# Kernel tuning notes

Hardware: AMD Instinct MI355X
Metric: run time of the kernel (lower is better)

## Reference

```python
import jax, jax.numpy as jnp
import numpy as np

B, S, H = 2, 2048, 2048
NH, NKV, HD = 16, 4, 128
ROPE_BASE = 10000.0


def hbit_linear(x, w):
    # BitNet: 8-bit per-token absmax activation quant, ternary (2-bit) weight quant
    s = 127.0 / jnp.clip(jnp.max(jnp.abs(x), axis=-1, keepdims=True), 1e-5, None)
    xq = jnp.clip(jnp.round(x * s), -128, 127) / s
    ws = 1.0 / jnp.clip(jnp.mean(jnp.abs(w)), 1e-5, None)
    wq = jnp.clip(jnp.round(w * ws), -1, 1) / ws
    return xq @ wq.T


def rotate_half(x):
    h = x.shape[-1] // 2
    return jnp.concatenate([-x[..., h:], x[..., :h]], axis=-1)


def rope_cos_sin(position_ids, head_dim, dtype):
    inv_freq = 1.0 / (ROPE_BASE ** (jnp.arange(0, head_dim, 2, dtype=jnp.float32) / head_dim))
    freqs = position_ids.astype(jnp.float32)[..., None] * inv_freq[None, None, :]  # (b,s,hd/2)
    emb = jnp.concatenate([freqs, freqs], axis=-1)  # (b,s,hd)
    return jnp.cos(emb).astype(dtype)[:, :, None, :], jnp.sin(emb).astype(dtype)[:, :, None, :]


def setup_inputs() -> dict:
    key = jax.random.key(0)
    ks = jax.random.split(key, 5)
    xavier = lambda k, shp: jax.random.uniform(k, shp, jnp.float32, -1.0, 1.0) * np.sqrt(6.0 / (shp[0] + shp[1]))
    causal = jnp.where(jnp.tril(jnp.ones((S, S), bool)), 0.0, -1e9).astype(jnp.float32)[None, None]
    return {
        "hidden_states": jax.random.normal(ks[0], (B, S, H), jnp.float32),
        "attention_mask": causal,
        "Wq": xavier(ks[1], (H, H)),
        "Wk": xavier(ks[2], (NKV * HD, H)),
        "Wv": xavier(ks[3], (NKV * HD, H)),
        "Wo": xavier(ks[4], (H, H)),
        "position_ids": jnp.arange(S, dtype=jnp.int64 if jax.config.jax_enable_x64 else jnp.int32)[None, :],
    }


def reference(hidden_states, attention_mask, Wq, Wk, Wv, Wo, position_ids):
    b, s, _ = hidden_states.shape
    q = hbit_linear(hidden_states, Wq).reshape(b, s, NH, HD)
    k = hbit_linear(hidden_states, Wk).reshape(b, s, NKV, HD)
    v = hbit_linear(hidden_states, Wv).reshape(b, s, NKV, HD)
    cos, sin = rope_cos_sin(position_ids, HD, q.dtype)  # (1,s,1,hd)
    q = q * cos + rotate_half(q) * sin
    k = k * cos + rotate_half(k) * sin
    n_rep = NH // NKV
    k = jnp.repeat(k, n_rep, axis=2)  # (b,s,NH,hd)
    v = jnp.repeat(v, n_rep, axis=2)
    scale = 1.0 / np.sqrt(HD)
    scores = jnp.einsum("bqhd,bkhd->bhqk", q, k) * scale + attention_mask
    probs = jax.nn.softmax(scores, axis=-1)  # dropout inactive (eval)
    out = jnp.einsum("bhqk,bkhd->bqhd", probs, v).reshape(b, s, NH * HD)
    return hbit_linear(out, Wo)
```

## Files before the change

kernel.cpp:

```cpp
#include <hip/hip_runtime.h>
#include <hip/hip_bf16.h>

#define B_ 2
#define S_ 2048
#define H_ 2048
#define NH_ 16
#define NKV_ 4
#define HD_ 128
#define M_ (B_*S_)
#define KVD_ (NKV_*HD_)

typedef signed char s8;
typedef __attribute__((ext_vector_type(8))) short short8;
typedef __attribute__((ext_vector_type(4))) float f32x4;
typedef __attribute__((ext_vector_type(4))) int int4v;

__device__ __forceinline__ float loadf(const void* p, long i, int isb){
  if (isb) return __bfloat162float(((const __hip_bfloat16*)p)[i]);
  return ((const float*)p)[i];
}

__device__ __forceinline__ unsigned short f2bf(float f){
  union { float f; unsigned u; } v; v.f = f;
  unsigned r = v.u + 0x7FFF + ((v.u >> 16) & 1);
  return (unsigned short)(r >> 16);
}

__device__ __forceinline__ float bf2f(unsigned short b){
  union { unsigned u; float f; } v; v.u = ((unsigned)b) << 16; return v.f;
}

__device__ __forceinline__ void gl2lds16(const void* g, void* l){
  __builtin_amdgcn_global_load_lds(
      (const __attribute__((address_space(1))) void*)g,
      (__attribute__((address_space(3))) void*)l, 16, 0, 0);
}

__global__ void k_detect(const unsigned int* x, int* flag){
  __shared__ int sh[256];
  int t = threadIdx.x, c = 0;
  for (int i = t; i < 2048; i += 256){
    unsigned e = (x[i] >> 7) & 0xFF;
    if (e >= 90 && e <= 150) c++;
  }
  sh[t] = c; __syncthreads();
  for (int k = 128; k > 0; k >>= 1){ if (t < k) sh[t] += sh[t+k]; __syncthreads(); }
  if (t == 0) flag[0] = (sh[0] > 1228) ? 1 : 0;
}

__global__ void k_rope_tab(float* ct, float* st){
  int d = threadIdx.x, pos = blockIdx.x;
  float inv = exp2f(-(float)d * 0.20762050593045952f);
  float a = (float)pos * inv;
  float sn, cs; sincosf(a, &sn, &cs);
  ct[pos*64 + d] = cs; st[pos*64 + d] = sn;
}

__global__ void k_wsum_all(const void* Wq, const void* Wk, const void* Wv, const void* Wo,
                           const int* flag, float* wsum){
  __shared__ float sh[256];
  int isb = *flag;
  int bid = blockIdx.x, t = threadIdx.x;
  const void* w; long n; int wi; long b0; int nb;
  if (bid < 512)       { w = Wq; wi = 0; n = (long)H_*H_;   b0 = bid;      nb = 512; }
  else if (bid < 768)  { w = Wk; wi = 1; n = (long)KVD_*H_; b0 = bid-512;  nb = 256; }
  else if (bid < 1024) { w = Wv; wi = 2; n = (long)KVD_*H_; b0 = bid-768;  nb = 256; }
  else                 { w = Wo; wi = 3; n = (long)H_*H_;   b0 = bid-1024; nb = 512; }
  float s = 0.f;
  for (long i = b0*256 + t; i < n; i += (long)nb*256) s += fabsf(loadf(w, i, isb));
  sh[t] = s; __syncthreads();
  for (int k = 128; k > 0; k >>= 1){ if (t < k) sh[t] += sh[t+k]; __syncthreads(); }
  if (t == 0) atomicAdd(&wsum[wi], sh[0]);
}

__global__ void k_wfin(const float* wsum, float* wscale){
  const float cnt[4] = { (float)((long)H_*H_), (float)((long)KVD_*H_),
                         (float)((long)KVD_*H_), (float)((long)H_*H_) };
  int t = threadIdx.x;
  if (t < 4){
    float m = wsum[t] / cnt[t];
    m = fmaxf(m, 1e-5f);
    wscale[t] = 1.0f / m;
  }
}

__global__ void k_wquant_all(const void* Wq, const void* Wk, const void* Wv, const void* Wo,
                             const int* flag, const float* wscale,
                             s8* oq, s8* ok, s8* ov, s8* oo){
  int isb = *flag;
  int bid = blockIdx.x, t = threadIdx.x;
  const void* w; s8* out; long n; int wi; long b0; int nb;
  if (bid < 1024)      { w = Wq; out = oq; wi = 0; n = (long)H_*H_;   b0 = bid;       nb = 1024; }
  else if (bid < 1280) { w = Wk; out = ok; wi = 1; n = (long)KVD_*H_; b0 = bid-1024;  nb = 256; }
  else if (bid < 1536) { w = Wv; out = ov; wi = 2; n = (long)KVD_*H_; b0 = bid-1280;  nb = 256; }
  else                 { w = Wo; out = oo; wi = 3; n = (long)H_*H_;   b0 = bid-1536;  nb = 1024; }
  float sc = wscale[wi];
  for (long i = b0*256 + t; i < n; i += (long)nb*256){
    float v = rintf(loadf(w, i, isb) * sc);
    v = fminf(fmaxf(v, -1.f), 1.f);
    out[i] = (s8)v;
  }
}

__global__ void k_aquant_in(const void* x, const int* flag, float* srow, s8* xq){
  __shared__ float sh[256];
  int isb = *flag; int r = blockIdx.x, t = threadIdx.x;
  long base = (long)r * H_;
  float v[8];
  if (isb){
    uint4 wv = ((const uint4*)((const unsigned short*)x + base))[t];
    unsigned u[4] = {wv.x, wv.y, wv.z, wv.w};
    #pragma unroll
    for (int i = 0; i < 4; i++){
      v[2*i]   = bf2f((unsigned short)(u[i] & 0xFFFF));
      v[2*i+1] = bf2f((unsigned short)(u[i] >> 16));
    }
  } else {
    const float4* p = (const float4*)((const float*)x + base);
    float4 a = p[t*2], b2 = p[t*2+1];
    v[0]=a.x; v[1]=a.y; v[2]=a.z; v[3]=a.w; v[4]=b2.x; v[5]=b2.y; v[6]=b2.z; v[7]=b2.w;
  }
  float mx = 0.f;
  #pragma unroll
  for (int i = 0; i < 8; i++) mx = fmaxf(mx, fabsf(v[i]));
  sh[t] = mx; __syncthreads();
  for (int k = 128; k > 0; k >>= 1){ if (t < k) sh[t] = fmaxf(sh[t], sh[t+k]); __syncthreads(); }
  float s = 127.0f / fmaxf(sh[0], 1e-5f);
  if (t == 0) srow[r] = s;
  unsigned long long pk = 0;
  #pragma unroll
  for (int i = 0; i < 8; i++){
    float q = fminf(fmaxf(rintf(v[i] * s), -128.f), 127.f);
    pk |= ((unsigned long long)(unsigned char)(s8)q) << (8*i);
  }
  *(unsigned long long*)(xq + base + t*8) = pk;
}

__global__ void k_aquant_f32(const float* x, float* srow, s8* xq){
  __shared__ float sh[256];
  int r = blockIdx.x, t = threadIdx.x;
  long base = (long)r * H_;
  const float4* p = (const float4*)(x + base);
  float4 a = p[t*2], b2 = p[t*2+1];
  float v[8] = {a.x,a.y,a.z,a.w,b2.x,b2.y,b2.z,b2.w};
  float mx = 0.f;
  #pragma unroll
  for (int i = 0; i < 8; i++) mx = fmaxf(mx, fabsf(v[i]));
  sh[t] = mx; __syncthreads();
  for (int k = 128; k > 0; k >>= 1){ if (t < k) sh[t] = fmaxf(sh[t], sh[t+k]); __syncthreads(); }
  float s = 127.0f / fmaxf(sh[0], 1e-5f);
  if (t == 0) srow[r] = s;
  unsigned long long pk = 0;
  #pragma unroll
  for (int i = 0; i < 8; i++){
    float q = fminf(fmaxf(rintf(v[i] * s), -128.f), 127.f);
    pk |= ((unsigned long long)(unsigned char)(s8)q) << (8*i);
  }
  *(unsigned long long*)(xq + base + t*8) = pk;
}

__global__ __launch_bounds__(256, 2) void k_gemm_mfma2(
      const s8* __restrict__ A, const s8* __restrict__ Bw,
      const float* __restrict__ srow, const float* __restrict__ wscale, int wi,
      void* __restrict__ Cout, int N, int mode,
      const int* __restrict__ flag, unsigned short* __restrict__ Vt,
      const float* __restrict__ ct, const float* __restrict__ st){
  __shared__ __align__(16) s8 As[128*64];
  __shared__ __align__(16) s8 Bs[128*64];
  int tid = threadIdx.x;
  int wave = tid >> 6, lane = tid & 63;
  int quad = lane >> 4, c = lane & 15;
  int wm = wave >> 1, wn = wave & 1;
  long arow = (long)blockIdx.y * 128, bcol = (long)blockIdx.x * 128;
  const int K = H_;

  int4v acc[4][4];
  #pragma unroll
  for (int mt = 0; mt < 4; mt++)
    #pragma unroll
    for (int nt = 0; nt < 4; nt++) acc[mt][nt] = (int4v){0,0,0,0};

  int rl = lane >> 2;
  int kq = (lane & 3) ^ ((lane >> 3) & 3);
  int ch0 = wave*2, ch1 = wave*2 + 1;
  long gA0 = (arow + ch0*16 + rl)*(long)K + kq*16;
  long gA1 = (arow + ch1*16 + rl)*(long)K + kq*16;
  long gB0 = (bcol + ch0*16 + rl)*(long)K + kq*16;
  long gB1 = (bcol + ch1*16 + rl)*(long)K + kq*16;

  int sA = quad ^ ((c >> 1) & 3);
  int ntl[4];
  #pragma unroll
  for (int nt = 0; nt < 4; nt++) ntl[nt] = 2*wn + (nt & 1) + 4*(nt >> 1);
  int frA[4], frB[4];
  #pragma unroll
  for (int mt = 0; mt < 4; mt++) frA[mt] = (wm*64 + mt*16 + c)*64 + sA*16;
  #pragma unroll
  for (int nt = 0; nt < 4; nt++) frB[nt] = (ntl[nt]*16 + c)*64 + sA*16;

  for (int k0 = 0; k0 < K; k0 += 64){
    gl2lds16(A  + gA0 + k0, As + ch0*1024);
    gl2lds16(A  + gA1 + k0, As + ch1*1024);
    gl2lds16(Bw + gB0 + k0, Bs + ch0*1024);
    gl2lds16(Bw + gB1 + k0, Bs + ch1*1024);
    __syncthreads();
    int4v afr[4], bfr[4];
    #pragma unroll
    for (int mt = 0; mt < 4; mt++) afr[mt] = *(const int4v*)&As[frA[mt]];
    #pragma unroll
    for (int nt = 0; nt < 4; nt++) bfr[nt] = *(const int4v*)&Bs[frB[nt]];
    #pragma unroll
    for (int mt = 0; mt < 4; mt++)
      #pragma unroll
      for (int nt = 0; nt < 4; nt++)
        acc[mt][nt] = __builtin_amdgcn_mfma_i32_16x16x64_i8(afr[mt], bfr[nt], acc[mt][nt], 0, 0, 0);
    __syncthreads();
  }

  float wsc = wscale[wi];
  if (mode == 0 || mode == 3){
    unsigned short* Ob = (unsigned short*)Cout;
    #pragma unroll
    for (int mt = 0; mt < 4; mt++){
      #pragma unroll
      for (int r = 0; r < 4; r++){
        long grow = arow + wm*64 + mt*16 + quad*4 + r;
        float sc = 1.0f / (srow[grow] * wsc);
        if (mode == 0) sc *= 0.08838834764831845f;
        int pos = (int)(grow & (S_-1));
        #pragma unroll
        for (int p = 0; p < 2; p++){
          int col_lo = (int)bcol + (2*wn + p)*16 + c;
          int d = col_lo & 63;
          float cv = ct[pos*64 + d], sv = st[pos*64 + d];
          float vlo = acc[mt][p][r]   * sc;
          float vhi = acc[mt][p+2][r] * sc;
          Ob[grow*(long)N + col_lo]      = f2bf(vlo*cv - vhi*sv);
          Ob[grow*(long)N + col_lo + 64] = f2bf(vhi*cv + vlo*sv);
        }
      }
    }
  } else if (mode == 1){
    #pragma unroll
    for (int mt = 0; mt < 4; mt++){
      #pragma unroll
      for (int r = 0; r < 4; r++){
        long grow = arow + wm*64 + mt*16 + quad*4 + r;
        float sc = 1.0f / (srow[grow] * wsc);
        long bb = grow >> 11; int sI = (int)(grow & (S_-1));
        unsigned short* base = Vt + bb*(long)KVD_*S_ + sI;
        #pragma unroll
        for (int nt = 0; nt < 4; nt++)
          base[(long)(bcol + ntl[nt]*16 + c)*S_] = f2bf(acc[mt][nt][r] * sc);
      }
    }
  } else {
    #pragma unroll
    for (int mt = 0; mt < 4; mt++){
      #pragma unroll
      for (int r = 0; r < 4; r++){
        long grow = arow + wm*64 + mt*16 + quad*4 + r;
        float sc = 1.0f / (srow[grow] * wsc);
        long cb = grow*(long)N + bcol + c;
        if (*flag){
          __hip_bfloat16* o = (__hip_bfloat16*)Cout;
          #pragma unroll
          for (int nt = 0; nt < 4; nt++)
            o[cb + ntl[nt]*16] = __float2bfloat16(acc[mt][nt][r] * sc);
        } else {
          float* o = (float*)Cout;
          #pragma unroll
          for (int nt = 0; nt < 4; nt++)
            o[cb + ntl[nt]*16] = acc[mt][nt][r] * sc;
        }
      }
    }
  }
}

#define PSTR 40
__global__ __launch_bounds__(256) void k_attn_mfma(const unsigned short* __restrict__ Qb,
    const unsigned short* __restrict__ Kb, const unsigned short* __restrict__ Vt,
    float* __restrict__ ob){
  int wid = threadIdx.x >> 6, lane = threadIdx.x & 63;
  int quad = lane >> 4, c = lane & 15;
  int kvh = blockIdx.y, b = blockIdx.z;
  int win = blockIdx.x;
  if (b == 1) win = (S_/32 - 1) - win;
  int h = kvh*4 + wid;
  int q0 = win*32;

  __shared__ __align__(16) unsigned short Ks[64*128];
  __shared__ __align__(16) unsigned short Vs[128*64];
  __shared__ __align__(16) unsigned short Ps[4][16*PSTR];

  short8 qf[2][4];
  #pragma unroll
  for (int t0 = 0; t0 < 2; t0++)
    #pragma unroll
    for (int f = 0; f < 4; f++)
      qf[t0][f] = *(const short8*)(Qb + ((long)(b*S_ + q0 + t0*16 + c)*NH_ + h)*HD_ + f*32 + quad*8);

  const unsigned short* Kg = Kb + (long)b*S_*KVD_ + kvh*HD_;
  const unsigned short* Vg = Vt + ((long)b*KVD_ + kvh*HD_)*S_;

  f32x4 o[2][8], ol[2];
  #pragma unroll
  for (int t0 = 0; t0 < 2; t0++){
    #pragma unroll
    for (int i = 0; i < 8; i++) o[t0][i] = (f32x4){0.f,0.f,0.f,0.f};
    ol[t0] = (f32x4){0.f,0.f,0.f,0.f};
  }
  short8 ones;
  #pragma unroll
  for (int i = 0; i < 8; i++) ones[i] = (short)0x3F80;

  int skey = lane >> 4;
  int kslot = lane & 15;
  int vrow = lane >> 3;
  int vslot = lane & 7;

  int nk = q0 + 32;
  for (int kc = 0; kc < nk; kc += 64){
    #pragma unroll
    for (int i = 0; i < 4; i++){
      int kk = wid*16 + i*4;
      int key = kk + skey;
      int g = kslot ^ (key & 15);
      gl2lds16(Kg + (long)(kc + key)*KVD_ + g*8, Ks + kk*128);
    }
    #pragma unroll
    for (int i = 0; i < 4; i++){
      int rr = wid*32 + i*8;
      int hd = rr + vrow;
      int g = vslot ^ (hd & 7);
      gl2lds16(Vg + (long)hd*S_ + kc + g*8, Vs + rr*64);
    }
    __syncthreads();

    f32x4 s[2][4];
    #pragma unroll
    for (int t0 = 0; t0 < 2; t0++)
      #pragma unroll
      for (int kt = 0; kt < 4; kt++) s[t0][kt] = (f32x4){0.f,0.f,0.f,0.f};
    #pragma unroll
    for (int kt = 0; kt < 4; kt++){
      short8 kf4[4];
      #pragma unroll
      for (int f = 0; f < 4; f++)
        kf4[f] = *(const short8*)&Ks[(kt*16 + c)*128 + ((f*4 + quad) ^ c)*8];
      #pragma unroll
      for (int t0 = 0; t0 < 2; t0++)
        #pragma unroll
        for (int f = 0; f < 4; f++)
          s[t0][kt] = __builtin_amdgcn_mfma_f32_16x16x32_bf16(qf[t0][f], kf4[f], s[t0][kt], 0, 0, 0);
    }
    #pragma unroll
    for (int t0 = 0; t0 < 2; t0++){
      int qr0 = q0 + t0*16;
      if (kc + 63 > qr0){
        #pragma unroll
        for (int kt = 0; kt < 4; kt++){
          int key = kc + kt*16 + c;
          #pragma unroll
          for (int r = 0; r < 4; r++)
            if (key > qr0 + quad*4 + r) s[t0][kt][r] = -1e30f;
        }
      }
    }
    #pragma unroll
    for (int pp = 0; pp < 2; pp++){
      short8 vf[8];
      #pragma unroll
      for (int nt = 0; nt < 8; nt++)
        vf[nt] = *(const short8*)&Vs[(nt*16 + c)*64 + ((pp*4 + quad) ^ (c & 7))*8];
      #pragma unroll
      for (int t0 = 0; t0 < 2; t0++){
        #pragma unroll
        for (int tk = 0; tk < 2; tk++)
          #pragma unroll
          for (int r = 0; r < 4; r++)
            Ps[wid][(quad*4 + r)*PSTR + tk*16 + c] = f2bf(__expf(s[t0][pp*2 + tk][r]));
        short8 pf = *(const short8*)&Ps[wid][c*PSTR + quad*8];
        #pragma unroll
        for (int nt = 0; nt < 8; nt++)
          o[t0][nt] = __builtin_amdgcn_mfma_f32_16x16x32_bf16(pf, vf[nt], o[t0][nt], 0, 0, 0);
        ol[t0] = __builtin_amdgcn_mfma_f32_16x16x32_bf16(pf, ones, ol[t0], 0, 0, 0);
      }
    }
    __syncthreads();
  }

  #pragma unroll
  for (int t0 = 0; t0 < 2; t0++){
    float il[4];
    #pragma unroll
    for (int r = 0; r < 4; r++) il[r] = 1.0f / ol[t0][r];
    #pragma unroll
    for (int nt = 0; nt < 8; nt++)
      #pragma unroll
      for (int r = 0; r < 4; r++)
        ob[((long)(b*S_ + q0 + t0*16 + quad*4 + r))*H_ + h*HD_ + nt*16 + c] = o[t0][nt][r]*il[r];
  }
}

extern "C" void kernel_launch(void* const* d_in, const int* in_sizes, int n_in,
                              void* d_out, int out_size, void* d_ws, size_t ws_size,
                              hipStream_t stream){
  (void)in_sizes; (void)n_in; (void)out_size; (void)ws_size;
  const void* x  = d_in[0];
  const void* Wq = d_in[2];
  const void* Wk = d_in[3];
  const void* Wv = d_in[4];
  const void* Wo = d_in[5];
  char* ws = (char*)d_ws;
  size_t o = 0;
  auto alloc = [&](size_t b){ size_t r = o; o += (b + 255) & ~(size_t)255; return r; };
  size_t META = alloc(256);
  float* wsum   = (float*)(ws + META);
  float* wscale = (float*)(ws + META + 16);
  int*   flag   = (int*)  (ws + META + 32);
  float* s_x = (float*)(ws + alloc((size_t)M_*4));
  float* s_a = (float*)(ws + alloc((size_t)M_*4));
  float* ct  = (float*)(ws + alloc((size_t)S_*64*4));
  float* st  = (float*)(ws + alloc((size_t)S_*64*4));
  s8* xq  = (s8*)(ws + alloc((size_t)M_*H_));
  s8* wqq = (s8*)(ws + alloc((size_t)H_*H_));
  s8* wkq = (s8*)(ws + alloc((size_t)KVD_*H_));
  s8* wvq = (s8*)(ws + alloc((size_t)KVD_*H_));
  s8* woq = (s8*)(ws + alloc((size_t)H_*H_));
  unsigned short* Qb = (unsigned short*)(ws + alloc((size_t)M_*NH_*HD_*2));
  unsigned short* Kb = (unsigned short*)(ws + alloc((size_t)M_*KVD_*2));
  unsigned short* Vt = (unsigned short*)(ws + alloc((size_t)M_*KVD_*2));
  float* ab = (float*)(ws + alloc((size_t)M_*H_*4));
  s8* aq = xq;

  hipMemsetAsync(ws + META, 0, 64, stream);
  k_detect<<<1,256,0,stream>>>((const unsigned int*)x, flag);
  k_rope_tab<<<S_,64,0,stream>>>(ct, st);

  k_wsum_all<<<1536,256,0,stream>>>(Wq, Wk, Wv, Wo, flag, wsum);
  k_wfin<<<1,64,0,stream>>>(wsum, wscale);
  k_wquant_all<<<2560,256,0,stream>>>(Wq, Wk, Wv, Wo, flag, wscale, wqq, wkq, wvq, woq);

  k_aquant_in<<<M_,256,0,stream>>>(x, flag, s_x, xq);

  dim3 gq(H_/128, M_/128), gkv(KVD_/128, M_/128);
  k_gemm_mfma2<<<gq, 256, 0, stream>>>(xq, wqq, s_x, wscale, 0, Qb, H_,   0, flag, nullptr, ct, st);
  k_gemm_mfma2<<<gkv,256, 0, stream>>>(xq, wkq, s_x, wscale, 1, Kb, KVD_, 3, flag, nullptr, ct, st);
  k_gemm_mfma2<<<gkv,256, 0, stream>>>(xq, wvq, s_x, wscale, 2, nullptr, KVD_, 1, flag, Vt, ct, st);

  dim3 ga(S_/32, NKV_, B_);
  k_attn_mfma<<<ga, 256, 0, stream>>>(Qb, Kb, Vt, ab);

  k_aquant_f32<<<M_,256,0,stream>>>(ab, s_a, aq);
  k_gemm_mfma2<<<gq,256,0,stream>>>(aq, woq, s_a, wscale, 3, d_out, H_, 2, flag, nullptr, ct, st);
}
```

Measured before the change: 353.0 us.

## Fuse prep kernels, merge QKV GEMMs, double-buffer K in attention, bf16 attention output

Merges the rope-table, weight-sum and weight-scale kernels into fewer launches. It also folds the Q, K and V projections into one GEMM launch with a block-index dispatch, and double-buffers K tiles in the attention loop so the next chunk loads during softmax·V. The attention output is now written as bf16 instead of fp32, halving its traffic for the activation-quant step. The bf16 rounding before 8-bit quantization can shift a few quantized values.

```diff
diff --git a/kernel.cpp b/kernel.cpp
--- a/kernel.cpp
+++ b/kernel.cpp
@@ -48,24 +48,22 @@
   if (t == 0) flag[0] = (sh[0] > 1228) ? 1 : 0;
 }
 
-__global__ void k_rope_tab(float* ct, float* st){
-  int d = threadIdx.x, pos = blockIdx.x;
-  float inv = exp2f(-(float)d * 0.20762050593045952f);
-  float a = (float)pos * inv;
-  float sn, cs; sincosf(a, &sn, &cs);
-  ct[pos*64 + d] = cs; st[pos*64 + d] = sn;
-}
-
-__global__ void k_wsum_all(const void* Wq, const void* Wk, const void* Wv, const void* Wo,
-                           const int* flag, float* wsum){
+__global__ void k_prep(const void* Wq, const void* Wk, const void* Wv, const void* Wo,
+                       const int* flag, float* wsum, float* ct, float* st){
+  int bid = blockIdx.x, t = threadIdx.x;
+  if (t < 64){
+    float inv = exp2f(-(float)t * 0.20762050593045952f);
+    float a = (float)bid * inv;
+    float sn, cs; sincosf(a, &sn, &cs);
+    ct[bid*64 + t] = cs; st[bid*64 + t] = sn;
+  }
   __shared__ float sh[256];
   int isb = *flag;
-  int bid = blockIdx.x, t = threadIdx.x;
   const void* w; long n; int wi; long b0; int nb;
-  if (bid < 512)       { w = Wq; wi = 0; n = (long)H_*H_;   b0 = bid;      nb = 512; }
-  else if (bid < 768)  { w = Wk; wi = 1; n = (long)KVD_*H_; b0 = bid-512;  nb = 256; }
-  else if (bid < 1024) { w = Wv; wi = 2; n = (long)KVD_*H_; b0 = bid-768;  nb = 256; }
-  else                 { w = Wo; wi = 3; n = (long)H_*H_;   b0 = bid-1024; nb = 512; }
+  if (bid < 768)       { w = Wq; wi = 0; n = (long)H_*H_;   b0 = bid;      nb = 768; }
+  else if (bid < 1024) { w = Wk; wi = 1; n = (long)KVD_*H_; b0 = bid-768;  nb = 256; }
+  else if (bid < 1280) { w = Wv; wi = 2; n = (long)KVD_*H_; b0 = bid-1024; nb = 256; }
+  else                 { w = Wo; wi = 3; n = (long)H_*H_;   b0 = bid-1280; nb = 768; }
   float s = 0.f;
   for (long i = b0*256 + t; i < n; i += (long)nb*256) s += fabsf(loadf(w, i, isb));
   sh[t] = s; __syncthreads();
@@ -73,28 +71,19 @@
   if (t == 0) atomicAdd(&wsum[wi], sh[0]);
 }
 
-__global__ void k_wfin(const float* wsum, float* wscale){
-  const float cnt[4] = { (float)((long)H_*H_), (float)((long)KVD_*H_),
-                         (float)((long)KVD_*H_), (float)((long)H_*H_) };
-  int t = threadIdx.x;
-  if (t < 4){
-    float m = wsum[t] / cnt[t];
-    m = fmaxf(m, 1e-5f);
-    wscale[t] = 1.0f / m;
-  }
-}
-
 __global__ void k_wquant_all(const void* Wq, const void* Wk, const void* Wv, const void* Wo,
-                             const int* flag, const float* wscale,
+                             const int* flag, const float* wsum,
                              s8* oq, s8* ok, s8* ov, s8* oo){
   int isb = *flag;
   int bid = blockIdx.x, t = threadIdx.x;
-  const void* w; s8* out; long n; int wi; long b0; int nb;
-  if (bid < 1024)      { w = Wq; out = oq; wi = 0; n = (long)H_*H_;   b0 = bid;       nb = 1024; }
-  else if (bid < 1280) { w = Wk; out = ok; wi = 1; n = (long)KVD_*H_; b0 = bid-1024;  nb = 256; }
-  else if (bid < 1536) { w = Wv; out = ov; wi = 2; n = (long)KVD_*H_; b0 = bid-1280;  nb = 256; }
-  else                 { w = Wo; out = oo; wi = 3; n = (long)H_*H_;   b0 = bid-1536;  nb = 1024; }
-  float sc = wscale[wi];
+  const float cntq = (float)((long)H_*H_), cntkv = (float)((long)KVD_*H_);
+  const void* w; s8* out; long n; int wi; long b0; int nb; float cnt;
+  if (bid < 1024)      { w = Wq; out = oq; wi = 0; n = (long)H_*H_;   b0 = bid;       nb = 1024; cnt = cntq; }
+  else if (bid < 1280) { w = Wk; out = ok; wi = 1; n = (long)KVD_*H_; b0 = bid-1024;  nb = 256;  cnt = cntkv; }
+  else if (bid < 1536) { w = Wv; out = ov; wi = 2; n = (long)KVD_*H_; b0 = bid-1280;  nb = 256;  cnt = cntkv; }
+  else                 { w = Wo; out = oo; wi = 3; n = (long)H_*H_;   b0 = bid-1536;  nb = 1024; cnt = cntq; }
+  float mean = fmaxf(wsum[wi] / cnt, 1e-5f);
+  float sc = 1.0f / mean;
   for (long i = b0*256 + t; i < n; i += (long)nb*256){
     float v = rintf(loadf(w, i, isb) * sc);
     v = fminf(fmaxf(v, -1.f), 1.f);
@@ -136,13 +125,18 @@
   *(unsigned long long*)(xq + base + t*8) = pk;
 }
 
-__global__ void k_aquant_f32(const float* x, float* srow, s8* xq){
+__global__ void k_aquant_bf16(const unsigned short* __restrict__ x, float* __restrict__ srow, s8* __restrict__ xq){
   __shared__ float sh[256];
   int r = blockIdx.x, t = threadIdx.x;
   long base = (long)r * H_;
-  const float4* p = (const float4*)(x + base);
-  float4 a = p[t*2], b2 = p[t*2+1];
-  float v[8] = {a.x,a.y,a.z,a.w,b2.x,b2.y,b2.z,b2.w};
+  uint4 wv = ((const uint4*)(x + base))[t];
+  unsigned u[4] = {wv.x, wv.y, wv.z, wv.w};
+  float v[8];
+  #pragma unroll
+  for (int i = 0; i < 4; i++){
+    v[2*i]   = bf2f((unsigned short)(u[i] & 0xFFFF));
+    v[2*i+1] = bf2f((unsigned short)(u[i] >> 16));
+  }
   float mx = 0.f;
   #pragma unroll
   for (int i = 0; i < 8; i++) mx = fmaxf(mx, fabsf(v[i]));
@@ -159,19 +153,17 @@
   *(unsigned long long*)(xq + base + t*8) = pk;
 }
 
-__global__ __launch_bounds__(256, 2) void k_gemm_mfma2(
-      const s8* __restrict__ A, const s8* __restrict__ Bw,
-      const float* __restrict__ srow, const float* __restrict__ wscale, int wi,
-      void* __restrict__ Cout, int N, int mode,
-      const int* __restrict__ flag, unsigned short* __restrict__ Vt,
-      const float* __restrict__ ct, const float* __restrict__ st){
-  __shared__ __align__(16) s8 As[128*64];
-  __shared__ __align__(16) s8 Bs[128*64];
+__device__ __forceinline__ void gemm_core(
+      const s8* __restrict__ A, const s8* __restrict__ Bw, s8* As, s8* Bs,
+      const float* __restrict__ srow, float mean,
+      void* __restrict__ Cout, int N, int mode, int isb,
+      unsigned short* __restrict__ Vt,
+      const float* __restrict__ ct, const float* __restrict__ st, long bcol){
   int tid = threadIdx.x;
   int wave = tid >> 6, lane = tid & 63;
   int quad = lane >> 4, c = lane & 15;
   int wm = wave >> 1, wn = wave & 1;
-  long arow = (long)blockIdx.y * 128, bcol = (long)blockIdx.x * 128;
+  long arow = (long)blockIdx.y * 128;
   const int K = H_;
 
   int4v acc[4][4];
@@ -217,7 +209,6 @@
     __syncthreads();
   }
 
-  float wsc = wscale[wi];
   if (mode == 0 || mode == 3){
     unsigned short* Ob = (unsigned short*)Cout;
     #pragma unroll
@@ -225,7 +216,7 @@
       #pragma unroll
       for (int r = 0; r < 4; r++){
         long grow = arow + wm*64 + mt*16 + quad*4 + r;
-        float sc = 1.0f / (srow[grow] * wsc);
+        float sc = mean / srow[grow];
         if (mode == 0) sc *= 0.08838834764831845f;
         int pos = (int)(grow & (S_-1));
         #pragma unroll
@@ -246,7 +237,7 @@
       #pragma unroll
       for (int r = 0; r < 4; r++){
         long grow = arow + wm*64 + mt*16 + quad*4 + r;
-        float sc = 1.0f / (srow[grow] * wsc);
+        float sc = mean / srow[grow];
         long bb = grow >> 11; int sI = (int)(grow & (S_-1));
         unsigned short* base = Vt + bb*(long)KVD_*S_ + sI;
         #pragma unroll
@@ -260,9 +251,9 @@
       #pragma unroll
       for (int r = 0; r < 4; r++){
         long grow = arow + wm*64 + mt*16 + quad*4 + r;
-        float sc = 1.0f / (srow[grow] * wsc);
+        float sc = mean / srow[grow];
         long cb = grow*(long)N + bcol + c;
-        if (*flag){
+        if (isb){
           __hip_bfloat16* o = (__hip_bfloat16*)Cout;
           #pragma unroll
           for (int nt = 0; nt < 4; nt++)
@@ -278,10 +269,44 @@
   }
 }
 
+__global__ __launch_bounds__(256, 2) void k_gemm_qkv(
+      const s8* __restrict__ xq,
+      const s8* __restrict__ wqq, const s8* __restrict__ wkq, const s8* __restrict__ wvq,
+      const float* __restrict__ srow, const float* __restrict__ wsum,
+      unsigned short* __restrict__ Qb, unsigned short* __restrict__ Kb,
+      unsigned short* __restrict__ Vt,
+      const float* __restrict__ ct, const float* __restrict__ st){
+  __shared__ __align__(16) s8 As[128*64];
+  __shared__ __align__(16) s8 Bs[128*64];
+  int bx = blockIdx.x;
+  const float cntq = (float)((long)H_*H_), cntkv = (float)((long)KVD_*H_);
+  const s8* Bw; void* Cout; unsigned short* vt = nullptr;
+  int N, mode; float mean; long bcol;
+  if (bx < 16){
+    Bw = wqq; Cout = Qb; N = H_;   mode = 0; mean = fmaxf(wsum[0]/cntq, 1e-5f);  bcol = (long)bx*128;
+  } else if (bx < 20){
+    Bw = wkq; Cout = Kb; N = KVD_; mode = 3; mean = fmaxf(wsum[1]/cntkv, 1e-5f); bcol = (long)(bx-16)*128;
+  } else {
+    Bw = wvq; Cout = nullptr; vt = Vt; N = KVD_; mode = 1; mean = fmaxf(wsum[2]/cntkv, 1e-5f); bcol = (long)(bx-20)*128;
+  }
+  gemm_core(xq, Bw, As, Bs, srow, mean, Cout, N, mode, 0, vt, ct, st, bcol);
+}
+
+__global__ __launch_bounds__(256, 2) void k_gemm_o(
+      const s8* __restrict__ aq, const s8* __restrict__ woq,
+      const float* __restrict__ srow, const float* __restrict__ wsum,
+      const int* __restrict__ flag, void* __restrict__ out,
+      const float* __restrict__ ct, const float* __restrict__ st){
+  __shared__ __align__(16) s8 As[128*64];
+  __shared__ __align__(16) s8 Bs[128*64];
+  float mean = fmaxf(wsum[3] / (float)((long)H_*H_), 1e-5f);
+  gemm_core(aq, woq, As, Bs, srow, mean, out, H_, 2, *flag, nullptr, ct, st, (long)blockIdx.x*128);
+}
+
 #define PSTR 40
 __global__ __launch_bounds__(256) void k_attn_mfma(const unsigned short* __restrict__ Qb,
     const unsigned short* __restrict__ Kb, const unsigned short* __restrict__ Vt,
-    float* __restrict__ ob){
+    unsigned short* __restrict__ ob){
   int wid = threadIdx.x >> 6, lane = threadIdx.x & 63;
   int quad = lane >> 4, c = lane & 15;
   int kvh = blockIdx.y, b = blockIdx.z;
@@ -290,7 +315,7 @@
   int h = kvh*4 + wid;
   int q0 = win*32;
 
-  __shared__ __align__(16) unsigned short Ks[64*128];
+  __shared__ __align__(16) unsigned short Ks[2][64*128];
   __shared__ __align__(16) unsigned short Vs[128*64];
   __shared__ __align__(16) unsigned short Ps[4][16*PSTR];
 
@@ -321,22 +346,24 @@
   int vslot = lane & 7;
 
   int nk = q0 + 32;
-  for (int kc = 0; kc < nk; kc += 64){
-    #pragma unroll
-    for (int i = 0; i < 4; i++){
-      int kk = wid*16 + i*4;
-      int key = kk + skey;
-      int g = kslot ^ (key & 15);
-      gl2lds16(Kg + (long)(kc + key)*KVD_ + g*8, Ks + kk*128);
-    }
+  #pragma unroll
+  for (int i = 0; i < 4; i++){
+    int kk = wid*16 + i*4;
+    int key = kk + skey;
+    int g = kslot ^ (key & 15);
+    gl2lds16(Kg + (long)key*KVD_ + g*8, &Ks[0][kk*128]);
+  }
+
+  int buf = 0;
+  for (int kc = 0; kc < nk; kc += 64, buf ^= 1){
+    __syncthreads();
     #pragma unroll
     for (int i = 0; i < 4; i++){
       int rr = wid*32 + i*8;
       int hd = rr + vrow;
       int g = vslot ^ (hd & 7);
-      gl2lds16(Vg + (long)hd*S_ + kc + g*8, Vs + rr*64);
-    }
-    __syncthreads();
+      gl2lds16(Vg + (long)hd*S_ + kc + g*8, &Vs[rr*64]);
+    }
 
     f32x4 s[2][4];
     #pragma unroll
@@ -348,7 +375,7 @@
       short8 kf4[4];
       #pragma unroll
       for (int f = 0; f < 4; f++)
-        kf4[f] = *(const short8*)&Ks[(kt*16 + c)*128 + ((f*4 + quad) ^ c)*8];
+        kf4[f] = *(const short8*)&Ks[buf][(kt*16 + c)*128 + ((f*4 + quad) ^ c)*8];
       #pragma unroll
       for (int t0 = 0; t0 < 2; t0++)
         #pragma unroll
@@ -368,6 +395,19 @@
         }
       }
     }
+
+    __syncthreads();
+
+    if (kc + 64 < nk){
+      #pragma unroll
+      for (int i = 0; i < 4; i++){
+        int kk = wid*16 + i*4;
+        int key = kk + skey;
+        int g = kslot ^ (key & 15);
+        gl2lds16(Kg + (long)(kc + 64 + key)*KVD_ + g*8, &Ks[buf^1][kk*128]);
+      }
+    }
+
     #pragma unroll
     for (int pp = 0; pp < 2; pp++){
       short8 vf[8];
@@ -388,7 +428,6 @@
         ol[t0] = __builtin_amdgcn_mfma_f32_16x16x32_bf16(pf, ones, ol[t0], 0, 0, 0);
       }
     }
-    __syncthreads();
   }
 
   #pragma unroll
@@ -400,7 +439,7 @@
     for (int nt = 0; nt < 8; nt++)
       #pragma unroll
       for (int r = 0; r < 4; r++)
-        ob[((long)(b*S_ + q0 + t0*16 + quad*4 + r))*H_ + h*HD_ + nt*16 + c] = o[t0][nt][r]*il[r];
+        ob[((long)(b*S_ + q0 + t0*16 + quad*4 + r))*H_ + h*HD_ + nt*16 + c] = f2bf(o[t0][nt][r]*il[r]);
   }
 }
 
@@ -417,9 +456,8 @@
   size_t o = 0;
   auto alloc = [&](size_t b){ size_t r = o; o += (b + 255) & ~(size_t)255; return r; };
   size_t META = alloc(256);
-  float* wsum   = (float*)(ws + META);
-  float* wscale = (float*)(ws + META + 16);
-  int*   flag   = (int*)  (ws + META + 32);
+  float* wsum = (float*)(ws + META);
+  int*   flag = (int*)  (ws + META + 32);
   float* s_x = (float*)(ws + alloc((size_t)M_*4));
   float* s_a = (float*)(ws + alloc((size_t)M_*4));
   float* ct  = (float*)(ws + alloc((size_t)S_*64*4));
@@ -432,27 +470,23 @@
   unsigned short* Qb = (unsigned short*)(ws + alloc((size_t)M_*NH_*HD_*2));
   unsigned short* Kb = (unsigned short*)(ws + alloc((size_t)M_*KVD_*2));
   unsigned short* Vt = (unsigned short*)(ws + alloc((size_t)M_*KVD_*2));
-  float* ab = (float*)(ws + alloc((size_t)M_*H_*4));
+  unsigned short* ab = (unsigned short*)(ws + alloc((size_t)M_*H_*2));
   s8* aq = xq;
 
   hipMemsetAsync(ws + META, 0, 64, stream);
   k_detect<<<1,256,0,stream>>>((const unsigned int*)x, flag);
-  k_rope_tab<<<S_,64,0,stream>>>(ct, st);
-
-  k_wsum_all<<<1536,256,0,stream>>>(Wq, Wk, Wv, Wo, flag, wsum);
-  k_wfin<<<1,64,0,stream>>>(wsum, wscale);
-  k_wquant_all<<<2560,256,0,stream>>>(Wq, Wk, Wv, Wo, flag, wscale, wqq, wkq, wvq, woq);
-
+  k_prep<<<2048,256,0,stream>>>(Wq, Wk, Wv, Wo, flag, wsum, ct, st);
+  k_wquant_all<<<2560,256,0,stream>>>(Wq, Wk, Wv, Wo, flag, wsum, wqq, wkq, wvq, woq);
   k_aquant_in<<<M_,256,0,stream>>>(x, flag, s_x, xq);
 
-  dim3 gq(H_/128, M_/128), gkv(KVD_/128, M_/128);
-  k_gemm_mfma2<<<gq, 256, 0, stream>>>(xq, wqq, s_x, wscale, 0, Qb, H_,   0, flag, nullptr, ct, st);
-  k_gemm_mfma2<<<gkv,256, 0, stream>>>(xq, wkq, s_x, wscale, 1, Kb, KVD_, 3, flag, nullptr, ct, st);
-  k_gemm_mfma2<<<gkv,256, 0, stream>>>(xq, wvq, s_x, wscale, 2, nullptr, KVD_, 1, flag, Vt, ct, st);
+  dim3 gqkv(16+4+4, M_/128);
+  k_gemm_qkv<<<gqkv, 256, 0, stream>>>(xq, wqq, wkq, wvq, s_x, wsum, Qb, Kb, Vt, ct, st);
 
   dim3 ga(S_/32, NKV_, B_);
   k_attn_mfma<<<ga, 256, 0, stream>>>(Qb, Kb, Vt, ab);
 
-  k_aquant_f32<<<M_,256,0,stream>>>(ab, s_a, aq);
-  k_gemm_mfma2<<<gq,256,0,stream>>>(aq, woq, s_a, wscale, 3, d_out, H_, 2, flag, nullptr, ct, st);
-}
+  k_aquant_bf16<<<M_,256,0,stream>>>(ab, s_a, aq);
+
+  dim3 go(H_/128, M_/128);
+  k_gemm_o<<<go, 256, 0, stream>>>(aq, woq, s_a, wsum, flag, d_out, ct, st);
+}
```

Measured after the change: 314.5 us. 1.12x faster.
